# Optimization experiments

Measured on AMD Instinct MI355X. Metric: run time of the kernel, lower is better.

The kernel has to match this reference:

```python
import math
import jax, jax.numpy as jnp
import numpy as np

D_MODEL = 1024
N_HEADS = 16
D_K = D_MODEL // N_HEADS


def setup_inputs() -> dict:
    key = jax.random.key(0)
    ks = jax.random.split(key, 10)
    s = 1.0 / math.sqrt(D_MODEL)
    return {
        "x": jax.random.normal(ks[0], (4, 4096, D_MODEL), dtype=jnp.float32),
        "memory_key": jax.random.normal(ks[1], (4, 4096, D_MODEL), dtype=jnp.float32),
        "Wq": jax.random.normal(ks[2], (D_MODEL, D_MODEL), dtype=jnp.float32) * s,
        "bq": jnp.zeros((D_MODEL,), dtype=jnp.float32),
        "Wk": jax.random.normal(ks[3], (D_MODEL, D_MODEL), dtype=jnp.float32) * s,
        "bk": jnp.zeros((D_MODEL,), dtype=jnp.float32),
        "Wv": jax.random.normal(ks[4], (D_MODEL, D_MODEL), dtype=jnp.float32) * s,
        "bv": jnp.zeros((D_MODEL,), dtype=jnp.float32),
        "Wo": jax.random.normal(ks[5], (D_MODEL, D_MODEL), dtype=jnp.float32) * s,
        "bo": jnp.zeros((D_MODEL,), dtype=jnp.float32),
    }


def _heads(t, b, n):
    # [b, n, d_model] -> [b, h, n, d_k]
    return t.reshape(b, n, N_HEADS, D_K).transpose(0, 2, 1, 3)


def reference(x, memory_key, Wq, bq, Wk, bk, Wv, bv, Wo, bo):
    b, n, _ = x.shape
    scale = 1.0 / math.sqrt(D_K)
    q = _heads(x @ Wq + bq, b, n)
    k = _heads(x @ Wk + bk, b, n)
    v = _heads(x @ Wv + bv, b, n)
    # feature-dim softmax (over d_k), scaled by 1/sqrt(d_k)
    q_soft = jax.nn.softmax(q * scale, axis=-1)
    k_soft = jax.nn.softmax(k * scale, axis=-1)
    kv = jnp.einsum('bhnd,bhne->bhde', k_soft, v)   # [b,h,d_k,d_k]
    out = jnp.einsum('bhnd,bhde->bhne', q_soft, kv)
    # memory path: softmax over reshaped memory_key heads, same value tensor
    m_soft = jax.nn.softmax(_heads(memory_key, b, n) * scale, axis=-1)
    mv = jnp.einsum('bhnd,bhne->bhde', m_soft, v)
    out = out + jnp.einsum('bhnd,bhde->bhne', q_soft, mv)
    out = out.transpose(0, 2, 1, 3).reshape(b, n, D_MODEL)
    # dropout is identity in eval mode
    return out @ Wo + bo
```

## Files before the change

### kernel.cpp

```cpp
#include <hip/hip_runtime.h>
#include <stdint.h>

typedef unsigned int uint;
typedef unsigned short ushort;
typedef __attribute__((ext_vector_type(4))) float  f32x4;
typedef __attribute__((ext_vector_type(8))) __bf16 bf16x8;

#define SCALE 0.125f

__device__ __forceinline__ ushort f2bf(float f) {
  uint u = __builtin_bit_cast(uint, f);
  u += 0x7FFFu + ((u >> 16) & 1u);
  return (ushort)(u >> 16);
}
__device__ __forceinline__ uint pack2bf(float a, float b) {
  return (uint)f2bf(a) | ((uint)f2bf(b) << 16);
}
__device__ __forceinline__ float bflo(uint u) { return __builtin_bit_cast(float, u << 16); }
__device__ __forceinline__ float bfhi(uint u) { return __builtin_bit_cast(float, u & 0xFFFF0000u); }

__device__ __forceinline__ void gload_lds16(const void* g, void* l) {
  __builtin_amdgcn_global_load_lds((const __attribute__((address_space(1))) void*)g,
                                   (__attribute__((address_space(3))) void*)l, 16, 0, 0);
}


__global__ __launch_bounds__(256) void cvt_all_kernel(
    const float4* __restrict__ x, uint2* __restrict__ xb,
    const float* __restrict__ Wq, const float* __restrict__ Wk, const float* __restrict__ Wv,
    ushort* __restrict__ WT) {
  __shared__ float tile[32][33];
  int bx = blockIdx.x;
  if (bx < 2048) {
    int i = bx * 256 + threadIdx.x;
    #pragma unroll
    for (int k = 0; k < 8; ++k) {
      int idx = i + k * 524288;
      float4 f = x[idx];
      xb[idx] = make_uint2(pack2bf(f.x, f.y), pack2bf(f.z, f.w));
    }
  } else {
    int lin = bx - 2048;
    int mat = lin >> 10;
    int rem = lin & 1023;
    int cb = rem & 31, rb = rem >> 5;
    const float* W = (mat == 0) ? Wq : (mat == 1) ? Wk : Wv;
    int tx = threadIdx.x & 31, ty = threadIdx.x >> 5;
    int c0 = cb * 32, r0 = rb * 32;
    #pragma unroll
    for (int i = 0; i < 4; ++i)
      tile[ty + i*8][tx] = W[(size_t)(r0 + ty + i*8) * 1024 + c0 + tx];
    __syncthreads();
    #pragma unroll
    for (int i = 0; i < 4; ++i)
      WT[(size_t)(mat*1024 + c0 + ty + i*8) * 1024 + r0 + tx] = f2bf(tile[tx][ty + i*8]);
  }
}

template<typename CT>
__device__ __forceinline__ void gemm_body(
    const ushort* __restrict__ A, const ushort* __restrict__ B, CT* __restrict__ C,
    int K, int ldc,
    const float* __restrict__ bias0, const float* __restrict__ bias1, const float* __restrict__ bias2,
    int b_batch_stride) {
  __shared__ ushort As[128 * 64];
  __shared__ ushort Bs[128 * 64];
  const int t = threadIdx.x;
  const int w = t >> 6, l = t & 63;
  const int wr = w >> 1, wc = w & 1;
  const int m0 = blockIdx.x * 128;
  const int n0 = blockIdx.y * 128;
  const ushort* Ap = A + (size_t)m0 * K;
  const ushort* Bp = B + (size_t)(m0 >> 12) * b_batch_stride + (size_t)n0 * K;

  f32x4 acc[4][4];
  const f32x4 zf = {0.f, 0.f, 0.f, 0.f};
  #pragma unroll
  for (int i = 0; i < 4; ++i)
    #pragma unroll
    for (int j = 0; j < 4; ++j) acc[i][j] = zf;

  const int lr = l & 15, lg = l >> 4;

  for (int kt = 0; kt < K; kt += 64) {
    #pragma unroll
    for (int i = 0; i < 4; ++i) {
      int gb = w * 64 + i * 256;
      int g  = gb + l;
      int row = g >> 3, c16 = g & 7;
      gload_lds16(Ap + (size_t)row * K + kt + c16 * 8, (void*)(As + gb * 8));
      gload_lds16(Bp + (size_t)row * K + kt + c16 * 8, (void*)(Bs + gb * 8));
    }
    __syncthreads();
    #pragma unroll
    for (int kk = 0; kk < 64; kk += 32) {
      bf16x8 a[4], b[4];
      #pragma unroll
      for (int m = 0; m < 4; ++m)
        a[m] = *(const bf16x8*)(As + (wr*64 + m*16 + lr) * 64 + kk + lg * 8);
      #pragma unroll
      for (int n = 0; n < 4; ++n)
        b[n] = *(const bf16x8*)(Bs + (wc*64 + n*16 + lr) * 64 + kk + lg * 8);
      #pragma unroll
      for (int m = 0; m < 4; ++m)
        #pragma unroll
        for (int n = 0; n < 4; ++n)
          acc[m][n] = __builtin_amdgcn_mfma_f32_16x16x32_bf16(a[m], b[n], acc[m][n], 0, 0, 0);
    }
    __syncthreads();
  }

  const float* bp = (n0 < 1024) ? bias0 : (n0 < 2048) ? bias1 : bias2;
  #pragma unroll
  for (int n = 0; n < 4; ++n) {
    int col = n0 + wc*64 + n*16 + lr;
    float bv = bp[col & 1023];
    #pragma unroll
    for (int m = 0; m < 4; ++m) {
      #pragma unroll
      for (int j = 0; j < 4; ++j) {
        int row = m0 + wr*64 + m*16 + lg*4 + j;
        float v = acc[m][n][j] + bv;
        if constexpr (sizeof(CT) == 2) C[(size_t)row * ldc + col] = (CT)f2bf(v);
        else                           C[(size_t)row * ldc + col] = v;
      }
    }
  }
}

__global__ __launch_bounds__(256, 2) void gemm1_qkv(
    const ushort* __restrict__ A, const ushort* __restrict__ B, ushort* __restrict__ C,
    const float* __restrict__ bq, const float* __restrict__ bk, const float* __restrict__ bv) {
  gemm_body<ushort>(A, B, C, 1024, 3072, bq, bk, bv, 0);
}

__global__ __launch_bounds__(256, 2) void gemm2_out(
    const ushort* __restrict__ A, const ushort* __restrict__ B, float* __restrict__ C,
    const float* __restrict__ bo) {
  gemm_body<float>(A, B, C, 1024, 1024, bo, bo, bo, 1024 * 1024);
}


__device__ __forceinline__ void unpack8(uint4 u, float s, float* x) {
  x[0]=bflo(u.x)*s; x[1]=bfhi(u.x)*s; x[2]=bflo(u.y)*s; x[3]=bfhi(u.y)*s;
  x[4]=bflo(u.z)*s; x[5]=bfhi(u.z)*s; x[6]=bflo(u.w)*s; x[7]=bfhi(u.w)*s;
}

__device__ __forceinline__ void softmax16_nomax(float* x) {
  float s = 0.f;
  #pragma unroll
  for (int i = 0; i < 16; ++i) { x[i] = __expf(x[i]); s += x[i]; }
  s += __shfl_xor(s, 1);
  s += __shfl_xor(s, 2);
  float inv = 1.f / s;
  #pragma unroll
  for (int i = 0; i < 16; ++i) x[i] *= inv;
}

__global__ __launch_bounds__(256) void softmax_qkm(
    const ushort* __restrict__ QKV, const float* __restrict__ mk,
    ushort* __restrict__ qs, ushort* __restrict__ wbuf) {
  int bid = blockIdx.x;
  bool kmode = bid >= 4096;
  int cb = kmode ? bid - 4096 : bid;
  int t = threadIdx.x;
  int cid = cb * 64 + (t >> 2);
  int sub = t & 3;
  int row = cid >> 4, h = cid & 15;
  int col0 = h * 64 + sub * 16;

  if (!kmode) {
    const uint4* p = (const uint4*)(QKV + (size_t)row * 3072 + col0);
    float x[16];
    unpack8(p[0], SCALE, x);
    unpack8(p[1], SCALE, x + 8);
    softmax16_nomax(x);
    uint4 o0 = make_uint4(pack2bf(x[0],x[1]), pack2bf(x[2],x[3]), pack2bf(x[4],x[5]), pack2bf(x[6],x[7]));
    uint4 o1 = make_uint4(pack2bf(x[8],x[9]), pack2bf(x[10],x[11]), pack2bf(x[12],x[13]), pack2bf(x[14],x[15]));
    uint4* q = (uint4*)(qs + (size_t)row * 1024 + col0);
    q[0] = o0; q[1] = o1;
  } else {
    const uint4* p = (const uint4*)(QKV + (size_t)row * 3072 + 1024 + col0);
    float ks[16];
    unpack8(p[0], SCALE, ks);
    unpack8(p[1], SCALE, ks + 8);
    softmax16_nomax(ks);
    const float4* mp = (const float4*)(mk + (size_t)row * 1024 + col0);
    float ms[16];
    #pragma unroll
    for (int i = 0; i < 4; ++i) {
      float4 f = mp[i];
      ms[i*4+0] = f.x * SCALE; ms[i*4+1] = f.y * SCALE;
      ms[i*4+2] = f.z * SCALE; ms[i*4+3] = f.w * SCALE;
    }
    softmax16_nomax(ms);
    #pragma unroll
    for (int i = 0; i < 16; ++i) ks[i] += ms[i];
    uint4 o0 = make_uint4(pack2bf(ks[0],ks[1]), pack2bf(ks[2],ks[3]), pack2bf(ks[4],ks[5]), pack2bf(ks[6],ks[7]));
    uint4 o1 = make_uint4(pack2bf(ks[8],ks[9]), pack2bf(ks[10],ks[11]), pack2bf(ks[12],ks[13]), pack2bf(ks[14],ks[15]));
    uint4* q = (uint4*)(wbuf + (size_t)row * 1024 + col0);
    q[0] = o0; q[1] = o1;
  }
}


__global__ __launch_bounds__(256) void kv_accum(
    const ushort* __restrict__ wbuf, const ushort* __restrict__ QKV, float* __restrict__ S) {
  __shared__ ushort Ws[128 * 64];
  __shared__ ushort Vs[128 * 64];
  int bx = blockIdx.x;
  int bh = bx >> 5, nc = bx & 31;
  int b = bh >> 4, h = bh & 15;
  int row0 = b * 4096 + nc * 128;
  int t = threadIdx.x, w = t >> 6, l = t & 63;
  #pragma unroll
  for (int i = 0; i < 4; ++i) {
    int gb = w * 64 + i * 256, g = gb + l;
    int r = g >> 3, c16 = g & 7;
    gload_lds16(wbuf + (size_t)(row0 + r) * 1024 + h * 64 + c16 * 8, (void*)(Ws + gb * 8));
    gload_lds16(QKV  + (size_t)(row0 + r) * 3072 + 2048 + h * 64 + c16 * 8, (void*)(Vs + gb * 8));
  }
  __syncthreads();
  int d0 = (t & 15) * 4, e0 = (t >> 4) * 4;
  float acc[4][4] = {};
  #pragma unroll 4
  for (int n = 0; n < 128; ++n) {
    uint2 wp = *(const uint2*)(Ws + n * 64 + d0);
    uint2 vp = *(const uint2*)(Vs + n * 64 + e0);
    float wd[4] = { bflo(wp.x), bfhi(wp.x), bflo(wp.y), bfhi(wp.y) };
    float vd[4] = { bflo(vp.x), bfhi(vp.x), bflo(vp.y), bfhi(vp.y) };
    #pragma unroll
    for (int i = 0; i < 4; ++i)
      #pragma unroll
      for (int j = 0; j < 4; ++j) acc[i][j] += wd[i] * vd[j];
  }
  float* Sp = S + (size_t)bh * 4096;
  #pragma unroll
  for (int i = 0; i < 4; ++i)
    #pragma unroll
    for (int j = 0; j < 4; ++j)
      atomicAdd(Sp + (d0 + i) * 64 + e0 + j, acc[i][j]);
}


__global__ __launch_bounds__(256) void make_w2t(
    const float* __restrict__ S, const float* __restrict__ Wo, ushort* __restrict__ W2T) {
  int bx = blockIdx.x;
  int b = bx >> 8, h = (bx >> 4) & 15, ot = (bx >> 2) & 3, it = bx & 3;
  int t = threadIdx.x;
  __shared__ float Ss[16 * 64];
  const float* Sp = S + (size_t)(b * 16 + h) * 4096 + it * 1024;
  #pragma unroll
  for (int i = 0; i < 4; ++i) Ss[t + i * 256] = Sp[t + i * 256];
  __syncthreads();
  int o = ot * 256 + t;
  float acc[16] = {};
  for (int e = 0; e < 64; ++e) {
    float wo = Wo[(size_t)(h * 64 + e) * 1024 + o];
    #pragma unroll
    for (int i = 0; i < 16; ++i) acc[i] += Ss[i * 64 + e] * wo;
  }
  ushort* dst = W2T + (size_t)(b * 1024 + o) * 1024 + h * 64 + it * 16;
  #pragma unroll
  for (int i = 0; i < 16; ++i) dst[i] = f2bf(acc[i]);
}


extern "C" void kernel_launch(void* const* d_in, const int* in_sizes, int n_in,
                              void* d_out, int out_size, void* d_ws, size_t ws_size,
                              hipStream_t stream) {
  const float* x  = (const float*)d_in[0];
  const float* mk = (const float*)d_in[1];
  const float* Wq = (const float*)d_in[2];
  const float* bq = (const float*)d_in[3];
  const float* Wk = (const float*)d_in[4];
  const float* bk = (const float*)d_in[5];
  const float* Wv = (const float*)d_in[6];
  const float* bv = (const float*)d_in[7];
  const float* Wo = (const float*)d_in[8];
  const float* bo = (const float*)d_in[9];
  float* out = (float*)d_out;

  char* ws = (char*)d_ws;
  ushort* xb    = (ushort*)(ws);
  ushort* wqkvT = (ushort*)(ws +  33554432);
  ushort* QKV   = (ushort*)(ws +  39845888);
  ushort* qs    = (ushort*)(ws + 140509184);
  ushort* wbuf  = (ushort*)(ws + 174063616);
  float*  S     = (float* )(ws + 207618048);
  ushort* W2T   = (ushort*)(ws + 208666624);

  cvt_all_kernel<<<5120, 256, 0, stream>>>((const float4*)x, (uint2*)xb, Wq, Wk, Wv, wqkvT);
  gemm1_qkv<<<dim3(128, 24), 256, 0, stream>>>(xb, wqkvT, QKV, bq, bk, bv);
  softmax_qkm<<<8192, 256, 0, stream>>>(QKV, mk, qs, wbuf);
  hipMemsetAsync(S, 0, 64 * 4096 * sizeof(float), stream);
  kv_accum<<<2048, 256, 0, stream>>>(wbuf, QKV, S);
  make_w2t<<<1024, 256, 0, stream>>>(S, Wo, W2T);
  gemm2_out<<<dim3(128, 8), 256, 0, stream>>>(qs, W2T, out, bo);
}
```

Baseline: 370.9 us.

## Fuse Q softmax into QKV GEMM epilogue and K/memory softmax into kv accumulation

The Q feature softmax moves into the QKV GEMM epilogue, using shuffle reductions across the 16 lanes of each head row, so qs is written directly and Q is no longer stored to QKV. The K and memory-key softmaxes are computed inside the kv accumulation kernel and written to a swizzled LDS tile, which removes the separate softmax kernel and the wbuf round trip. The memset of S is folded into extra blocks of the conversion kernel. This saves two launches and a large intermediate read/write, at the cost of heavier per-thread register use in kv_fused and scattered 2-byte stores in the GEMM epilogue.

```diff
diff --git a/kernel.cpp b/kernel.cpp
--- a/kernel.cpp
+++ b/kernel.cpp
@@ -24,11 +24,16 @@
                                    (__attribute__((address_space(3))) void*)l, 16, 0, 0);
 }
 
+__device__ __forceinline__ void unpack8(uint4 u, float s, float* x) {
+  x[0]=bflo(u.x)*s; x[1]=bfhi(u.x)*s; x[2]=bflo(u.y)*s; x[3]=bfhi(u.y)*s;
+  x[4]=bflo(u.z)*s; x[5]=bfhi(u.z)*s; x[6]=bflo(u.w)*s; x[7]=bfhi(u.w)*s;
+}
+
 
 __global__ __launch_bounds__(256) void cvt_all_kernel(
     const float4* __restrict__ x, uint2* __restrict__ xb,
     const float* __restrict__ Wq, const float* __restrict__ Wk, const float* __restrict__ Wv,
-    ushort* __restrict__ WT) {
+    ushort* __restrict__ WT, float4* __restrict__ S4) {
   __shared__ float tile[32][33];
   int bx = blockIdx.x;
   if (bx < 2048) {
@@ -39,7 +44,7 @@
       float4 f = x[idx];
       xb[idx] = make_uint2(pack2bf(f.x, f.y), pack2bf(f.z, f.w));
     }
-  } else {
+  } else if (bx < 5120) {
     int lin = bx - 2048;
     int mat = lin >> 10;
     int rem = lin & 1023;
@@ -54,24 +59,29 @@
     #pragma unroll
     for (int i = 0; i < 4; ++i)
       WT[(size_t)(mat*1024 + c0 + ty + i*8) * 1024 + r0 + tx] = f2bf(tile[tx][ty + i*8]);
-  }
-}
-
-template<typename CT>
-__device__ __forceinline__ void gemm_body(
-    const ushort* __restrict__ A, const ushort* __restrict__ B, CT* __restrict__ C,
-    int K, int ldc,
-    const float* __restrict__ bias0, const float* __restrict__ bias1, const float* __restrict__ bias2,
-    int b_batch_stride) {
+  } else {
+    int base = ((bx - 5120) * 256 + threadIdx.x) * 8;
+    const float4 z = {0.f, 0.f, 0.f, 0.f};
+    #pragma unroll
+    for (int j = 0; j < 8; ++j) S4[base + j] = z;
+  }
+}
+
+
+__global__ __launch_bounds__(256, 2) void gemm1_qkv(
+    const ushort* __restrict__ A, const ushort* __restrict__ B,
+    ushort* __restrict__ QKV, ushort* __restrict__ qs,
+    const float* __restrict__ bq, const float* __restrict__ bk, const float* __restrict__ bv) {
   __shared__ ushort As[128 * 64];
   __shared__ ushort Bs[128 * 64];
+  const int K = 1024;
   const int t = threadIdx.x;
   const int w = t >> 6, l = t & 63;
   const int wr = w >> 1, wc = w & 1;
   const int m0 = blockIdx.x * 128;
   const int n0 = blockIdx.y * 128;
   const ushort* Ap = A + (size_t)m0 * K;
-  const ushort* Bp = B + (size_t)(m0 >> 12) * b_batch_stride + (size_t)n0 * K;
+  const ushort* Bp = B + (size_t)n0 * K;
 
   f32x4 acc[4][4];
   const f32x4 zf = {0.f, 0.f, 0.f, 0.f};
@@ -110,122 +120,176 @@
     __syncthreads();
   }
 
-  const float* bp = (n0 < 1024) ? bias0 : (n0 < 2048) ? bias1 : bias2;
-  #pragma unroll
-  for (int n = 0; n < 4; ++n) {
-    int col = n0 + wc*64 + n*16 + lr;
-    float bv = bp[col & 1023];
+  if (n0 < 1024) {
+    const int cb = n0 + wc * 64;
+    float bvv[4];
+    #pragma unroll
+    for (int n = 0; n < 4; ++n) bvv[n] = bq[cb + n*16 + lr];
     #pragma unroll
     for (int m = 0; m < 4; ++m) {
       #pragma unroll
       for (int j = 0; j < 4; ++j) {
         int row = m0 + wr*64 + m*16 + lg*4 + j;
-        float v = acc[m][n][j] + bv;
-        if constexpr (sizeof(CT) == 2) C[(size_t)row * ldc + col] = (CT)f2bf(v);
-        else                           C[(size_t)row * ldc + col] = v;
+        float v[4];
+        float s = 0.f;
+        #pragma unroll
+        for (int n = 0; n < 4; ++n) {
+          v[n] = __expf((acc[m][n][j] + bvv[n]) * SCALE);
+          s += v[n];
+        }
+        s += __shfl_xor(s, 1);
+        s += __shfl_xor(s, 2);
+        s += __shfl_xor(s, 4);
+        s += __shfl_xor(s, 8);
+        float inv = 1.f / s;
+        #pragma unroll
+        for (int n = 0; n < 4; ++n)
+          qs[(size_t)row * 1024 + cb + n*16 + lr] = f2bf(v[n] * inv);
       }
     }
-  }
-}
-
-__global__ __launch_bounds__(256, 2) void gemm1_qkv(
-    const ushort* __restrict__ A, const ushort* __restrict__ B, ushort* __restrict__ C,
-    const float* __restrict__ bq, const float* __restrict__ bk, const float* __restrict__ bv) {
-  gemm_body<ushort>(A, B, C, 1024, 3072, bq, bk, bv, 0);
-}
+  } else {
+    const float* bp = (n0 < 2048) ? bk : bv;
+    #pragma unroll
+    for (int n = 0; n < 4; ++n) {
+      int col = n0 + wc*64 + n*16 + lr;
+      float bvv = bp[col & 1023];
+      #pragma unroll
+      for (int m = 0; m < 4; ++m) {
+        #pragma unroll
+        for (int j = 0; j < 4; ++j) {
+          int row = m0 + wr*64 + m*16 + lg*4 + j;
+          QKV[(size_t)row * 3072 + col] = f2bf(acc[m][n][j] + bvv);
+        }
+      }
+    }
+  }
+}
+
 
 __global__ __launch_bounds__(256, 2) void gemm2_out(
     const ushort* __restrict__ A, const ushort* __restrict__ B, float* __restrict__ C,
     const float* __restrict__ bo) {
-  gemm_body<float>(A, B, C, 1024, 1024, bo, bo, bo, 1024 * 1024);
-}
-
-
-__device__ __forceinline__ void unpack8(uint4 u, float s, float* x) {
-  x[0]=bflo(u.x)*s; x[1]=bfhi(u.x)*s; x[2]=bflo(u.y)*s; x[3]=bfhi(u.y)*s;
-  x[4]=bflo(u.z)*s; x[5]=bfhi(u.z)*s; x[6]=bflo(u.w)*s; x[7]=bfhi(u.w)*s;
-}
-
-__device__ __forceinline__ void softmax16_nomax(float* x) {
-  float s = 0.f;
-  #pragma unroll
-  for (int i = 0; i < 16; ++i) { x[i] = __expf(x[i]); s += x[i]; }
-  s += __shfl_xor(s, 1);
-  s += __shfl_xor(s, 2);
-  float inv = 1.f / s;
-  #pragma unroll
-  for (int i = 0; i < 16; ++i) x[i] *= inv;
-}
-
-__global__ __launch_bounds__(256) void softmax_qkm(
-    const ushort* __restrict__ QKV, const float* __restrict__ mk,
-    ushort* __restrict__ qs, ushort* __restrict__ wbuf) {
-  int bid = blockIdx.x;
-  bool kmode = bid >= 4096;
-  int cb = kmode ? bid - 4096 : bid;
-  int t = threadIdx.x;
-  int cid = cb * 64 + (t >> 2);
-  int sub = t & 3;
-  int row = cid >> 4, h = cid & 15;
-  int col0 = h * 64 + sub * 16;
-
-  if (!kmode) {
-    const uint4* p = (const uint4*)(QKV + (size_t)row * 3072 + col0);
-    float x[16];
-    unpack8(p[0], SCALE, x);
-    unpack8(p[1], SCALE, x + 8);
-    softmax16_nomax(x);
-    uint4 o0 = make_uint4(pack2bf(x[0],x[1]), pack2bf(x[2],x[3]), pack2bf(x[4],x[5]), pack2bf(x[6],x[7]));
-    uint4 o1 = make_uint4(pack2bf(x[8],x[9]), pack2bf(x[10],x[11]), pack2bf(x[12],x[13]), pack2bf(x[14],x[15]));
-    uint4* q = (uint4*)(qs + (size_t)row * 1024 + col0);
-    q[0] = o0; q[1] = o1;
-  } else {
-    const uint4* p = (const uint4*)(QKV + (size_t)row * 3072 + 1024 + col0);
-    float ks[16];
-    unpack8(p[0], SCALE, ks);
-    unpack8(p[1], SCALE, ks + 8);
-    softmax16_nomax(ks);
-    const float4* mp = (const float4*)(mk + (size_t)row * 1024 + col0);
-    float ms[16];
+  __shared__ ushort As[128 * 64];
+  __shared__ ushort Bs[128 * 64];
+  const int K = 1024;
+  const int t = threadIdx.x;
+  const int w = t >> 6, l = t & 63;
+  const int wr = w >> 1, wc = w & 1;
+  const int m0 = blockIdx.x * 128;
+  const int n0 = blockIdx.y * 128;
+  const ushort* Ap = A + (size_t)m0 * K;
+  const ushort* Bp = B + (size_t)(m0 >> 12) * (1024 * 1024) + (size_t)n0 * K;
+
+  f32x4 acc[4][4];
+  const f32x4 zf = {0.f, 0.f, 0.f, 0.f};
+  #pragma unroll
+  for (int i = 0; i < 4; ++i)
+    #pragma unroll
+    for (int j = 0; j < 4; ++j) acc[i][j] = zf;
+
+  const int lr = l & 15, lg = l >> 4;
+
+  for (int kt = 0; kt < K; kt += 64) {
     #pragma unroll
     for (int i = 0; i < 4; ++i) {
-      float4 f = mp[i];
-      ms[i*4+0] = f.x * SCALE; ms[i*4+1] = f.y * SCALE;
-      ms[i*4+2] = f.z * SCALE; ms[i*4+3] = f.w * SCALE;
-    }
-    softmax16_nomax(ms);
-    #pragma unroll
-    for (int i = 0; i < 16; ++i) ks[i] += ms[i];
-    uint4 o0 = make_uint4(pack2bf(ks[0],ks[1]), pack2bf(ks[2],ks[3]), pack2bf(ks[4],ks[5]), pack2bf(ks[6],ks[7]));
-    uint4 o1 = make_uint4(pack2bf(ks[8],ks[9]), pack2bf(ks[10],ks[11]), pack2bf(ks[12],ks[13]), pack2bf(ks[14],ks[15]));
-    uint4* q = (uint4*)(wbuf + (size_t)row * 1024 + col0);
-    q[0] = o0; q[1] = o1;
-  }
-}
-
-
-__global__ __launch_bounds__(256) void kv_accum(
-    const ushort* __restrict__ wbuf, const ushort* __restrict__ QKV, float* __restrict__ S) {
+      int gb = w * 64 + i * 256;
+      int g  = gb + l;
+      int row = g >> 3, c16 = g & 7;
+      gload_lds16(Ap + (size_t)row * K + kt + c16 * 8, (void*)(As + gb * 8));
+      gload_lds16(Bp + (size_t)row * K + kt + c16 * 8, (void*)(Bs + gb * 8));
+    }
+    __syncthreads();
+    #pragma unroll
+    for (int kk = 0; kk < 64; kk += 32) {
+      bf16x8 a[4], b[4];
+      #pragma unroll
+      for (int m = 0; m < 4; ++m)
+        a[m] = *(const bf16x8*)(As + (wr*64 + m*16 + lr) * 64 + kk + lg * 8);
+      #pragma unroll
+      for (int n = 0; n < 4; ++n)
+        b[n] = *(const bf16x8*)(Bs + (wc*64 + n*16 + lr) * 64 + kk + lg * 8);
+      #pragma unroll
+      for (int m = 0; m < 4; ++m)
+        #pragma unroll
+        for (int n = 0; n < 4; ++n)
+          acc[m][n] = __builtin_amdgcn_mfma_f32_16x16x32_bf16(a[m], b[n], acc[m][n], 0, 0, 0);
+    }
+    __syncthreads();
+  }
+
+  #pragma unroll
+  for (int n = 0; n < 4; ++n) {
+    int col = n0 + wc*64 + n*16 + lr;
+    float bvv = bo[col];
+    #pragma unroll
+    for (int m = 0; m < 4; ++m) {
+      #pragma unroll
+      for (int j = 0; j < 4; ++j) {
+        int row = m0 + wr*64 + m*16 + lg*4 + j;
+        C[(size_t)row * 1024 + col] = acc[m][n][j] + bvv;
+      }
+    }
+  }
+}
+
+
+__global__ __launch_bounds__(256) void kv_fused(
+    const ushort* __restrict__ QKV, const float* __restrict__ mk, float* __restrict__ S) {
+  __shared__ ushort Vs[128 * 64];
   __shared__ ushort Ws[128 * 64];
-  __shared__ ushort Vs[128 * 64];
   int bx = blockIdx.x;
   int bh = bx >> 5, nc = bx & 31;
   int b = bh >> 4, h = bh & 15;
   int row0 = b * 4096 + nc * 128;
   int t = threadIdx.x, w = t >> 6, l = t & 63;
+
   #pragma unroll
   for (int i = 0; i < 4; ++i) {
     int gb = w * 64 + i * 256, g = gb + l;
     int r = g >> 3, c16 = g & 7;
-    gload_lds16(wbuf + (size_t)(row0 + r) * 1024 + h * 64 + c16 * 8, (void*)(Ws + gb * 8));
-    gload_lds16(QKV  + (size_t)(row0 + r) * 3072 + 2048 + h * 64 + c16 * 8, (void*)(Vs + gb * 8));
+    gload_lds16(QKV + (size_t)(row0 + r) * 3072 + 2048 + h * 64 + c16 * 8, (void*)(Vs + gb * 8));
+  }
+
+  {
+    int r = t >> 1, hf = t & 1;
+    const uint4* kp = (const uint4*)(QKV + (size_t)(row0 + r) * 3072 + 1024 + h * 64 + hf * 32);
+    float ke[32], me[32];
+    #pragma unroll
+    for (int i = 0; i < 4; ++i) unpack8(kp[i], SCALE, ke + i * 8);
+    const float4* mp = (const float4*)(mk + (size_t)(row0 + r) * 1024 + h * 64 + hf * 32);
+    #pragma unroll
+    for (int i = 0; i < 8; ++i) {
+      float4 f = mp[i];
+      me[i*4+0] = f.x * SCALE; me[i*4+1] = f.y * SCALE;
+      me[i*4+2] = f.z * SCALE; me[i*4+3] = f.w * SCALE;
+    }
+    float ksum = 0.f, msum = 0.f;
+    #pragma unroll
+    for (int i = 0; i < 32; ++i) { ke[i] = __expf(ke[i]); ksum += ke[i]; }
+    #pragma unroll
+    for (int i = 0; i < 32; ++i) { me[i] = __expf(me[i]); msum += me[i]; }
+    ksum += __shfl_xor(ksum, 1);
+    msum += __shfl_xor(msum, 1);
+    float kinv = 1.f / ksum, minv = 1.f / msum;
+    #pragma unroll
+    for (int i = 0; i < 4; ++i) {
+      int gsw = (hf * 4 + i) ^ (r & 7);
+      uint4 o = make_uint4(
+        pack2bf(ke[i*8+0]*kinv + me[i*8+0]*minv, ke[i*8+1]*kinv + me[i*8+1]*minv),
+        pack2bf(ke[i*8+2]*kinv + me[i*8+2]*minv, ke[i*8+3]*kinv + me[i*8+3]*minv),
+        pack2bf(ke[i*8+4]*kinv + me[i*8+4]*minv, ke[i*8+5]*kinv + me[i*8+5]*minv),
+        pack2bf(ke[i*8+6]*kinv + me[i*8+6]*minv, ke[i*8+7]*kinv + me[i*8+7]*minv));
+      *(uint4*)(Ws + r * 64 + gsw * 8) = o;
+    }
   }
   __syncthreads();
+
   int d0 = (t & 15) * 4, e0 = (t >> 4) * 4;
+  const int gq = d0 >> 3, sub = d0 & 7;
   float acc[4][4] = {};
   #pragma unroll 4
   for (int n = 0; n < 128; ++n) {
-    uint2 wp = *(const uint2*)(Ws + n * 64 + d0);
+    uint2 wp = *(const uint2*)(Ws + n * 64 + ((gq ^ (n & 7)) << 3) + sub);
     uint2 vp = *(const uint2*)(Vs + n * 64 + e0);
     float wd[4] = { bflo(wp.x), bfhi(wp.x), bflo(wp.y), bfhi(wp.y) };
     float vd[4] = { bflo(vp.x), bfhi(vp.x), bflo(vp.y), bfhi(vp.y) };
@@ -286,15 +350,13 @@
   ushort* wqkvT = (ushort*)(ws +  33554432);
   ushort* QKV   = (ushort*)(ws +  39845888);
   ushort* qs    = (ushort*)(ws + 140509184);
-  ushort* wbuf  = (ushort*)(ws + 174063616);
   float*  S     = (float* )(ws + 207618048);
   ushort* W2T   = (ushort*)(ws + 208666624);
 
-  cvt_all_kernel<<<5120, 256, 0, stream>>>((const float4*)x, (uint2*)xb, Wq, Wk, Wv, wqkvT);
-  gemm1_qkv<<<dim3(128, 24), 256, 0, stream>>>(xb, wqkvT, QKV, bq, bk, bv);
-  softmax_qkm<<<8192, 256, 0, stream>>>(QKV, mk, qs, wbuf);
-  hipMemsetAsync(S, 0, 64 * 4096 * sizeof(float), stream);
-  kv_accum<<<2048, 256, 0, stream>>>(wbuf, QKV, S);
+  cvt_all_kernel<<<5152, 256, 0, stream>>>((const float4*)x, (uint2*)xb,
+                                           Wq, Wk, Wv, wqkvT, (float4*)S);
+  gemm1_qkv<<<dim3(128, 24), 256, 0, stream>>>(xb, wqkvT, QKV, qs, bq, bk, bv);
+  kv_fused<<<2048, 256, 0, stream>>>(QKV, mk, S);
   make_w2t<<<1024, 256, 0, stream>>>(S, Wo, W2T);
   gemm2_out<<<dim3(128, 8), 256, 0, stream>>>(qs, W2T, out, bo);
 }
```

After: 347.4 us. -6.3%, faster.
